# Optimization experiments

Measured on AMD Instinct MI355X. Metric: run time of the kernel, lower is better.

## Reference

```python
import jax, jax.numpy as jnp
import numpy as np

VEC = 64
HEADS = 16
DUP = 4
HIDDEN = VEC * HEADS * DUP  # 4096
EPS = 1e-12


def setup_inputs() -> dict:
    key = jax.random.key(0)
    ks = jax.random.split(key, 7)
    B, S, N = 4, 512, 512
    out_len = VEC * HEADS
    return {
        "embeddings": jax.random.normal(ks[0], (B, S, HIDDEN), jnp.float32),
        "keys": jax.random.normal(ks[1], (B, N, out_len), jnp.float32),
        "values": jax.random.normal(ks[2], (B, N, out_len), jnp.float32),
        "Wq": jax.random.normal(ks[3], (HIDDEN, HIDDEN), jnp.float32) * (1.0 / np.sqrt(HIDDEN)),
        "bq": jnp.zeros((HIDDEN,), jnp.float32),
        "Wre": jax.random.normal(ks[4], (HIDDEN, HIDDEN), jnp.float32) * (1.0 / np.sqrt(HIDDEN)),
        "bre": jnp.zeros((HIDDEN,), jnp.float32),
        "ln_g": jnp.ones((HIDDEN,), jnp.float32),
        "ln_b": jnp.zeros((HIDDEN,), jnp.float32),
    }


def reference(embeddings, keys, values, Wq, bq, Wre, bre, ln_g, ln_b):
    B, S, _ = embeddings.shape
    N = keys.shape[1]
    # query projection: (B,S,hidden) -> reshape to (B, S*DUP, VEC, HEADS) -> (B,H,S*DUP,VEC)
    q = embeddings @ Wq.T + bq
    q = q.reshape(B, S * DUP, VEC, HEADS).transpose(0, 3, 1, 2)
    # keys: (B,N,VEC*HEADS) -> (B,H,VEC,N); values -> (B,H,N,VEC)
    k = keys.reshape(B, N, VEC, HEADS).transpose(0, 3, 2, 1)
    v = values.reshape(B, N, VEC, HEADS).transpose(0, 3, 1, 2)
    scores = jnp.matmul(q, k) / np.sqrt(VEC).astype(np.float32)  # (B,H,S*DUP,N)
    probs = jax.nn.softmax(scores, axis=-1)
    out = jnp.matmul(probs, v)  # (B,H,S*DUP,VEC)
    # (B,H,S*DUP,VEC) -> (B,H,S,VEC*DUP) -> (B,S,H,VEC*DUP) -> (B,S,HIDDEN)
    out = out.reshape(B, HEADS, S, VEC * DUP).transpose(0, 2, 1, 3).reshape(B, S, HIDDEN)
    # LayerNorm (biased variance, torch semantics)
    mu = jnp.mean(out, axis=-1, keepdims=True)
    var = jnp.mean(jnp.square(out - mu), axis=-1, keepdims=True)
    ln = (out - mu) / jnp.sqrt(var + EPS) * ln_g + ln_b
    return ln @ Wre.T + bre
```

## Files before the change

kernel.cpp:

```cpp
#include <hip/hip_runtime.h>

typedef __attribute__((ext_vector_type(8))) _Float16 half8;
typedef __attribute__((ext_vector_type(4))) _Float16 half4;
typedef __attribute__((ext_vector_type(4))) float    floatx4;

#define GLD16(g, l)                                                            \
  __builtin_amdgcn_global_load_lds(                                            \
      (const __attribute__((address_space(1))) void*)(g),                      \
      (__attribute__((address_space(3))) void*)(l), 16, 0, 0)

#define MFMA16(a, b, c) __builtin_amdgcn_mfma_f32_16x16x32_f16(a, b, c, 0, 0, 0)

__device__ __forceinline__ void cvt8(const float* __restrict__ in,
                                     _Float16* __restrict__ out, int i) {
  const float4* p = (const float4*)in + (size_t)i * 2;
  float4 a = p[0], b = p[1];
  half8 h;
  h[0] = (_Float16)a.x; h[1] = (_Float16)a.y; h[2] = (_Float16)a.z; h[3] = (_Float16)a.w;
  h[4] = (_Float16)b.x; h[5] = (_Float16)b.y; h[6] = (_Float16)b.z; h[7] = (_Float16)b.w;
  *(half8*)(out + (size_t)i * 8) = h;
}

__global__ __launch_bounds__(256) void prepA(const float* __restrict__ emb,
                                             const float* __restrict__ Wq,
                                             const float* __restrict__ keys,
                                             const float* __restrict__ values,
                                             _Float16* __restrict__ embH,
                                             _Float16* __restrict__ WqH,
                                             _Float16* __restrict__ Kh,
                                             _Float16* __restrict__ Vt) {
  const int bid = blockIdx.x, t = threadIdx.x;
  if (bid < 4096) {
    cvt8(emb, embH, bid * 256 + t);
  } else if (bid < 12288) {
    cvt8(Wq, WqH, (bid - 4096) * 256 + t);
  } else {
    const int tid = (bid - 12288) * 256 + t;
    {
      int v = tid & 63, n = (tid >> 6) & 511, h = (tid >> 15) & 15, b = tid >> 19;
      Kh[tid] = (_Float16)keys[((size_t)(b * 512 + n)) * 1024 + v * 16 + h];
    }
    {
      int n = tid & 511, v = (tid >> 9) & 63, h = (tid >> 15) & 15, b = tid >> 19;
      Vt[tid] = (_Float16)values[((size_t)(b * 512 + n)) * 1024 + v * 16 + h];
    }
  }
}

template <int MODE>
__global__ __launch_bounds__(512, 2) void gemm_bt(const _Float16* __restrict__ A,
                                                  const _Float16* __restrict__ Bw,
                                                  const float* __restrict__ bias,
                                                  float* __restrict__ Cf,
                                                  _Float16* __restrict__ H0,
                                                  _Float16* __restrict__ H1) {
  const int K = 4096;
  const int NT = 32;
  __shared__ _Float16 lA[2 * 16384];
  __shared__ _Float16 lB[2 * 16384];
  const int t = threadIdx.x, lane = t & 63, w = t >> 6;
  const int m0 = blockIdx.y * 256, n0 = blockIdx.x * 256;
  const int kb = blockIdx.z * 2048;
  const int wm = (w >> 2) * 128, wn = (w & 3) * 64;
  const int fr = lane & 15, fq = lane >> 4;

  const int srow = t >> 3;
  const int sch = (t & 7) ^ (srow & 7);
  const _Float16* gA = A + (size_t)(m0 + srow) * K + kb + sch * 8;
  const _Float16* gB = Bw + (size_t)(n0 + srow) * K + kb + sch * 8;
  _Float16* dA = &lA[t * 8];
  _Float16* dB = &lB[t * 8];

#define STG(op, bf_, kt_, h_)                                                  \
  do {                                                                         \
    const _Float16* g_ = (op ? gB : gA) + (size_t)((h_)*128) * K + (kt_)*64;   \
    _Float16* d_ = (op ? dB : dA) + (bf_)*16384 + (h_)*8192;                   \
    GLD16(g_, d_);                                                             \
    GLD16(g_ + (size_t)64 * K, d_ + 4096);                                     \
  } while (0)

  STG(0, 0, 0, 0); STG(0, 0, 0, 1); STG(1, 0, 0, 0); STG(1, 0, 0, 1);
  STG(0, 1, 1, 0); STG(0, 1, 1, 1); STG(1, 1, 1, 0);
  asm volatile("s_waitcnt vmcnt(6)" ::: "memory");
  __builtin_amdgcn_s_barrier();

  floatx4 acc[8][4];
#pragma unroll
  for (int i = 0; i < 8; i++)
#pragma unroll
    for (int j = 0; j < 4; j++) acc[i][j] = (floatx4)(0.f);

  const _Float16* cA = lA + (wm + fr) * 64;
  const _Float16* cB = lB + (wn + fr) * 64;
  const int xo0 = ((fq) ^ (fr & 7)) * 8;
  const int xo1 = ((4 + fq) ^ (fr & 7)) * 8;

#define QUAD(ibase, jbase)                                                     \
  do {                                                                         \
    __builtin_amdgcn_s_setprio(1);                                             \
    _Pragma("unroll") for (int i_ = 0; i_ < 4; i_++) {                         \
      _Pragma("unroll") for (int jj_ = 0; jj_ < 2; jj_++) {                    \
        acc[(ibase) + i_][(jbase) + jj_] =                                     \
            MFMA16(af[(ibase) + i_][0], bf[jj_][0], acc[(ibase) + i_][(jbase) + jj_]); \
        acc[(ibase) + i_][(jbase) + jj_] =                                     \
            MFMA16(af[(ibase) + i_][1], bf[jj_][1], acc[(ibase) + i_][(jbase) + jj_]); \
      }                                                                        \
    }                                                                          \
    __builtin_amdgcn_s_setprio(0);                                             \
  } while (0)

#define TILE(BUF, TT)                                                          \
  do {                                                                         \
    const int kt1 = ((TT) + 1 < NT) ? (TT) + 1 : NT - 1;                       \
    const int kt2 = ((TT) + 2 < NT) ? (TT) + 2 : NT - 1;                       \
    const int o = (BUF)*16384;                                                 \
    half8 af[8][2], bf[2][2];                                                  \
                              \
    STG(1, (BUF) ^ 1, kt1, 1);                                                 \
    _Pragma("unroll") for (int i = 0; i < 4; i++) {                            \
      af[i][0] = *(const half8*)(cA + o + i * 1024 + xo0);                     \
      af[i][1] = *(const half8*)(cA + o + i * 1024 + xo1);                     \
    }                                                                          \
    _Pragma("unroll") for (int jj = 0; jj < 2; jj++) {                         \
      bf[jj][0] = *(const half8*)(cB + o + jj * 1024 + xo0);                   \
      bf[jj][1] = *(const half8*)(cB + o + jj * 1024 + xo1);                   \
    }                                                                          \
    QUAD(0, 0);                                                                \
    __builtin_amdgcn_s_barrier();                                              \
                                                     \
    _Pragma("unroll") for (int i = 4; i < 8; i++) {                            \
      af[i][0] = *(const half8*)(cA + o + i * 1024 + xo0);                     \
      af[i][1] = *(const half8*)(cA + o + i * 1024 + xo1);                     \
    }                                                                          \
    QUAD(4, 0);                                                                \
    __builtin_amdgcn_s_barrier();                                              \
                                    \
    STG(0, (BUF), kt2, 0);                                                     \
    bf[0][0] = *(const half8*)(cB + o + 2 * 1024 + xo0);                       \
    bf[0][1] = *(const half8*)(cB + o + 2 * 1024 + xo1);                       \
    bf[1][0] = *(const half8*)(cB + o + 3 * 1024 + xo0);                       \
    bf[1][1] = *(const half8*)(cB + o + 3 * 1024 + xo1);                       \
    QUAD(0, 2);                                                                \
    __builtin_amdgcn_s_barrier();                                              \
                        \
    STG(0, (BUF), kt2, 1);                                                     \
    STG(1, (BUF), kt2, 0);                                                     \
    QUAD(4, 2);                                                                \
    asm volatile("s_waitcnt vmcnt(6)" ::: "memory");                           \
    __builtin_amdgcn_s_barrier();                                              \
  } while (0)

  for (int tt = 0; tt < NT; tt += 2) {
    TILE(0, tt);
    TILE(1, tt + 1);
  }

  const int z = blockIdx.z;
#pragma unroll
  for (int i = 0; i < 8; i++)
#pragma unroll
    for (int j = 0; j < 4; j++) {
      const int col = n0 + wn + j * 16 + fr;
      const int rbase = m0 + wm + i * 16 + fq * 4;
      if (MODE == 0 && z == 0) {
        const float bv = bias[col];
#pragma unroll
        for (int r = 0; r < 4; r++)
          Cf[(size_t)(rbase + r) * 4096 + col] = acc[i][j][r] + bv;
      } else {
        _Float16* P = z ? H1 : H0;
#pragma unroll
        for (int r = 0; r < 4; r++)
          P[(size_t)(rbase + r) * 4096 + col] = (_Float16)acc[i][j][r];
      }
    }
#undef TILE
#undef QUAD
#undef STG
}

__global__ __launch_bounds__(256) void prepB(const float* __restrict__ Wre,
                                             _Float16* __restrict__ WreH,
                                             const _Float16* __restrict__ p0,
                                             const _Float16* __restrict__ p1,
                                             const float* __restrict__ bq,
                                             _Float16* __restrict__ q) {
  const int bid = blockIdx.x, t = threadIdx.x;
  if (bid < 8192) {
    cvt8(Wre, WreH, bid * 256 + t);
    return;
  }
  __shared__ _Float16 T[4][16][80];
  const int L = t & 63, w = t >> 6;
  const int m = bid - 8192, d = w;
  const int b = m >> 9, s = m & 511;
  const size_t src = (size_t)m * 4096 + d * 1024 + L * 16;
  half8 a0 = *(const half8*)(p0 + src);
  half8 a1 = *(const half8*)(p0 + src + 8);
  half8 b0 = *(const half8*)(p1 + src);
  half8 b1 = *(const half8*)(p1 + src + 8);
  const float4* bqv = (const float4*)(bq + d * 1024 + L * 16);
  float bias[16];
#pragma unroll
  for (int c = 0; c < 4; c++) {
    float4 f = bqv[c];
    bias[c * 4 + 0] = f.x; bias[c * 4 + 1] = f.y;
    bias[c * 4 + 2] = f.z; bias[c * 4 + 3] = f.w;
  }
#pragma unroll
  for (int h = 0; h < 8; h++) {
    T[w][h][L] = (_Float16)(((float)a0[h] + (float)b0[h] + bias[h]) * 0.125f);
    T[w][h + 8][L] =
        (_Float16)(((float)a1[h] + (float)b1[h] + bias[h + 8]) * 0.125f);
  }
  const int h2 = L >> 2, c2 = L & 3;
  _Float16* dst = q + (((size_t)(b * 16 + h2) * 2048) + s * 4 + d) * 64 + c2 * 8;
  *(half8*)dst = *(const half8*)&T[w][h2][c2 * 8];
  *(half8*)(dst + 32) = *(const half8*)&T[w][h2][32 + c2 * 8];
}

__global__ __launch_bounds__(256) void combine2(float* __restrict__ out,
                                                const _Float16* __restrict__ p1) {
  const int i4 = (blockIdx.x * 256 + threadIdx.x) * 4;
  float4 o = *(float4*)&out[i4];
  half4 p = *(const half4*)(p1 + i4);
  o.x += (float)p[0];
  o.y += (float)p[1];
  o.z += (float)p[2];
  o.w += (float)p[3];
  *(float4*)&out[i4] = o;
}

__global__ __launch_bounds__(256) void attn_mfma(const _Float16* __restrict__ Q,
                                                 const _Float16* __restrict__ Kh,
                                                 const _Float16* __restrict__ Vt,
                                                 float* __restrict__ Out) {
  __shared__ _Float16 Pbuf[4][32][136];
  const int t = threadIdx.x, lane = t & 63, w = t >> 6;
  const int fr = lane & 15, fq = lane >> 4;
  const int bh = blockIdx.y, qt = blockIdx.x;
  const int b = bh >> 4, h = bh & 15;

  const _Float16* Qb = Q + ((size_t)bh * 2048 + qt * 128 + w * 32) * 64;
  const _Float16* Kb = Kh + (size_t)bh * 512 * 64;
  const _Float16* Vb = Vt + (size_t)bh * 64 * 512;

  half8 qf[2][2];
#pragma unroll
  for (int i = 0; i < 2; i++)
#pragma unroll
    for (int ks = 0; ks < 2; ks++)
      qf[i][ks] = *(const half8*)(Qb + (i * 16 + fr) * 64 + ks * 32 + fq * 8);

  floatx4 oacc[2][4];
  float l_acc[2][4];
#pragma unroll
  for (int i = 0; i < 2; i++)
#pragma unroll
    for (int j = 0; j < 4; j++) {
      oacc[i][j] = (floatx4)(0.f);
      l_acc[i][j] = 0.f;
    }

  for (int c0 = 0; c0 < 512; c0 += 128) {
    floatx4 sc[2][8];
#pragma unroll
    for (int i = 0; i < 2; i++)
#pragma unroll
      for (int j = 0; j < 8; j++) sc[i][j] = (floatx4)(0.f);
#pragma unroll
    for (int j = 0; j < 8; j++) {
      const _Float16* kr = Kb + (size_t)(c0 + j * 16 + fr) * 64 + fq * 8;
      half8 k0 = *(const half8*)kr;
      half8 k1 = *(const half8*)(kr + 32);
#pragma unroll
      for (int i = 0; i < 2; i++) {
        sc[i][j] = __builtin_amdgcn_mfma_f32_16x16x32_f16(qf[i][0], k0, sc[i][j], 0, 0, 0);
        sc[i][j] = __builtin_amdgcn_mfma_f32_16x16x32_f16(qf[i][1], k1, sc[i][j], 0, 0, 0);
      }
    }
    half8 vr[4][4];
#pragma unroll
    for (int kn = 0; kn < 4; kn++)
#pragma unroll
      for (int jv = 0; jv < 4; jv++)
        vr[kn][jv] =
            *(const half8*)(Vb + (size_t)(jv * 16 + fr) * 512 + c0 + kn * 32 + fq * 8);
#pragma unroll
    for (int i = 0; i < 2; i++)
#pragma unroll
      for (int j = 0; j < 8; j++)
#pragma unroll
        for (int r = 0; r < 4; r++) {
          float p = __expf(sc[i][j][r]);
          l_acc[i][r] += p;
          Pbuf[w][i * 16 + fq * 4 + r][j * 16 + fr] = (_Float16)p;
        }
#pragma unroll
    for (int kn = 0; kn < 4; kn++) {
      half8 pa[2];
#pragma unroll
      for (int i = 0; i < 2; i++)
        pa[i] = *(const half8*)&Pbuf[w][i * 16 + fr][kn * 32 + fq * 8];
#pragma unroll
      for (int jv = 0; jv < 4; jv++) {
#pragma unroll
        for (int i = 0; i < 2; i++)
          oacc[i][jv] = __builtin_amdgcn_mfma_f32_16x16x32_f16(pa[i], vr[kn][jv],
                                                              oacc[i][jv], 0, 0, 0);
      }
    }
  }

#pragma unroll
  for (int i = 0; i < 2; i++)
#pragma unroll
    for (int r = 0; r < 4; r++) {
#pragma unroll
      for (int m = 8; m; m >>= 1)
        l_acc[i][r] += __shfl_xor(l_acc[i][r], m, 16);
    }
#pragma unroll
  for (int i = 0; i < 2; i++) {
#pragma unroll
    for (int r = 0; r < 4; r++) {
      const float inv = 1.f / l_acc[i][r];
      const int m2 = qt * 128 + w * 32 + i * 16 + fq * 4 + r;
      float* orow = Out + ((size_t)(b * 512 + (m2 >> 2))) * 4096 + h * 256 + (m2 & 3) * 64 + fr;
#pragma unroll
      for (int jv = 0; jv < 4; jv++) orow[jv * 16] = oacc[i][jv][r] * inv;
    }
  }
}

__global__ __launch_bounds__(256) void ln_kernel(const float* __restrict__ X,
                                                 const float* __restrict__ g,
                                                 const float* __restrict__ bb,
                                                 _Float16* __restrict__ Y) {
  const int row = blockIdx.x;
  const int t = threadIdx.x;
  const float* x = X + (size_t)row * 4096;
  float4 vals[4];
  float sum = 0.f, sq = 0.f;
#pragma unroll
  for (int c = 0; c < 4; c++) {
    vals[c] = *(const float4*)&x[c * 1024 + t * 4];
    sum += vals[c].x + vals[c].y + vals[c].z + vals[c].w;
    sq += vals[c].x * vals[c].x + vals[c].y * vals[c].y + vals[c].z * vals[c].z +
          vals[c].w * vals[c].w;
  }
#pragma unroll
  for (int off = 32; off > 0; off >>= 1) {
    sum += __shfl_down(sum, off, 64);
    sq += __shfl_down(sq, off, 64);
  }
  __shared__ float red[8];
  const int w = t >> 6;
  if ((t & 63) == 0) {
    red[w] = sum;
    red[4 + w] = sq;
  }
  __syncthreads();
  sum = red[0] + red[1] + red[2] + red[3];
  sq = red[4] + red[5] + red[6] + red[7];
  const float mu = sum * (1.f / 4096.f);
  float var = sq * (1.f / 4096.f) - mu * mu;
  var = fmaxf(var, 0.f);
  const float rstd = rsqrtf(var + 1e-12f);
#pragma unroll
  for (int c = 0; c < 4; c++) {
    const int j = c * 1024 + t * 4;
    float4 gg = *(const float4*)&g[j];
    float4 bv = *(const float4*)&bb[j];
    half4 y;
    y[0] = (_Float16)((vals[c].x - mu) * rstd * gg.x + bv.x);
    y[1] = (_Float16)((vals[c].y - mu) * rstd * gg.y + bv.y);
    y[2] = (_Float16)((vals[c].z - mu) * rstd * gg.z + bv.z);
    y[3] = (_Float16)((vals[c].w - mu) * rstd * gg.w + bv.w);
    *(half4*)&Y[(size_t)row * 4096 + j] = y;
  }
}

extern "C" void kernel_launch(void* const* d_in, const int* in_sizes, int n_in,
                              void* d_out, int out_size, void* d_ws,
                              size_t ws_size, hipStream_t stream) {
  const float* emb = (const float*)d_in[0];
  const float* keys = (const float*)d_in[1];
  const float* values = (const float*)d_in[2];
  const float* Wq = (const float*)d_in[3];
  const float* bq = (const float*)d_in[4];
  const float* Wre = (const float*)d_in[5];
  const float* bre = (const float*)d_in[6];
  const float* ln_g = (const float*)d_in[7];
  const float* ln_b = (const float*)d_in[8];
  float* out = (float*)d_out;

  char* ws = (char*)d_ws;
  _Float16* embH = (_Float16*)(ws);
  _Float16* WqH = (_Float16*)(ws + ((size_t)16 << 20));
  _Float16* Kh = (_Float16*)(ws + ((size_t)48 << 20));
  _Float16* Vt = (_Float16*)(ws + ((size_t)52 << 20));
  _Float16* P0q = (_Float16*)d_out;
  _Float16* P1q = (_Float16*)((char*)d_out + ((size_t)16 << 20));
  _Float16* WreH = WqH;
  _Float16* qattn = (_Float16*)(ws);
  _Float16* lnH = (_Float16*)(ws + ((size_t)48 << 20));
  _Float16* P1o = (_Float16*)(ws);

  prepA<<<20480, 256, 0, stream>>>(emb, Wq, keys, values, embH, WqH, Kh, Vt);
  gemm_bt<1><<<dim3(16, 8, 2), 512, 0, stream>>>(embH, WqH, nullptr, nullptr,
                                                 P0q, P1q);
  prepB<<<10240, 256, 0, stream>>>(Wre, WreH, P0q, P1q, bq, qattn);
  attn_mfma<<<dim3(16, 64), 256, 0, stream>>>(qattn, Kh, Vt, out);
  ln_kernel<<<2048, 256, 0, stream>>>(out, ln_g, ln_b, lnH);
  gemm_bt<0><<<dim3(16, 8, 2), 512, 0, stream>>>(lnH, WreH, bre, out, nullptr,
                                                 P1o);
  combine2<<<8192, 256, 0, stream>>>(out, P1o);
}
```

Measured before the change: 443.8 us.

## Replace split-K 256x256 GEMM with 128x128 tiles over full K

```diff
diff --git a/kernel.cpp b/kernel.cpp
--- a/kernel.cpp
+++ b/kernel.cpp
@@ -48,45 +48,41 @@
 }
 
 template <int MODE>
-__global__ __launch_bounds__(512, 2) void gemm_bt(const _Float16* __restrict__ A,
+__global__ __launch_bounds__(256, 2) void gemm_bt(const _Float16* __restrict__ A,
                                                   const _Float16* __restrict__ Bw,
                                                   const float* __restrict__ bias,
                                                   float* __restrict__ Cf,
-                                                  _Float16* __restrict__ H0,
-                                                  _Float16* __restrict__ H1) {
+                                                  _Float16* __restrict__ H0) {
   const int K = 4096;
-  const int NT = 32;
-  __shared__ _Float16 lA[2 * 16384];
-  __shared__ _Float16 lB[2 * 16384];
+  const int NT = 64;
+  __shared__ _Float16 lA[2 * 8192];
+  __shared__ _Float16 lB[2 * 8192];
   const int t = threadIdx.x, lane = t & 63, w = t >> 6;
-  const int m0 = blockIdx.y * 256, n0 = blockIdx.x * 256;
-  const int kb = blockIdx.z * 2048;
-  const int wm = (w >> 2) * 128, wn = (w & 3) * 64;
+  const int m0 = blockIdx.y * 128, n0 = blockIdx.x * 128;
+  const int wm = (w >> 1) * 64, wn = (w & 1) * 64;
   const int fr = lane & 15, fq = lane >> 4;
 
   const int srow = t >> 3;
   const int sch = (t & 7) ^ (srow & 7);
-  const _Float16* gA = A + (size_t)(m0 + srow) * K + kb + sch * 8;
-  const _Float16* gB = Bw + (size_t)(n0 + srow) * K + kb + sch * 8;
+  const _Float16* gA = A + (size_t)(m0 + srow) * K + sch * 8;
+  const _Float16* gB = Bw + (size_t)(n0 + srow) * K + sch * 8;
   _Float16* dA = &lA[t * 8];
   _Float16* dB = &lB[t * 8];
 
 #define STG(op, bf_, kt_, h_)                                                  \
-  do {                                                                         \
-    const _Float16* g_ = (op ? gB : gA) + (size_t)((h_)*128) * K + (kt_)*64;   \
-    _Float16* d_ = (op ? dB : dA) + (bf_)*16384 + (h_)*8192;                   \
-    GLD16(g_, d_);                                                             \
-    GLD16(g_ + (size_t)64 * K, d_ + 4096);                                     \
-  } while (0)
-
-  STG(0, 0, 0, 0); STG(0, 0, 0, 1); STG(1, 0, 0, 0); STG(1, 0, 0, 1);
-  STG(0, 1, 1, 0); STG(0, 1, 1, 1); STG(1, 1, 1, 0);
-  asm volatile("s_waitcnt vmcnt(6)" ::: "memory");
+  GLD16((op ? gB : gA) + (size_t)((h_)*32) * K + (kt_)*64,                     \
+        (op ? dB : dA) + (bf_)*8192 + (h_)*2048)
+
+  STG(0, 0, 0, 0); STG(0, 0, 0, 1); STG(0, 0, 0, 2); STG(0, 0, 0, 3);
+  STG(1, 0, 0, 0); STG(1, 0, 0, 1); STG(1, 0, 0, 2); STG(1, 0, 0, 3);
+  STG(0, 1, 1, 0); STG(0, 1, 1, 1); STG(0, 1, 1, 2); STG(0, 1, 1, 3);
+  STG(1, 1, 1, 0); STG(1, 1, 1, 1); STG(1, 1, 1, 2); STG(1, 1, 1, 3);
+  asm volatile("s_waitcnt vmcnt(8)" ::: "memory");
   __builtin_amdgcn_s_barrier();
 
-  floatx4 acc[8][4];
-#pragma unroll
-  for (int i = 0; i < 8; i++)
+  floatx4 acc[4][4];
+#pragma unroll
+  for (int i = 0; i < 4; i++)
 #pragma unroll
     for (int j = 0; j < 4; j++) acc[i][j] = (floatx4)(0.f);
 
@@ -98,12 +94,14 @@
 #define QUAD(ibase, jbase)                                                     \
   do {                                                                         \
     __builtin_amdgcn_s_setprio(1);                                             \
-    _Pragma("unroll") for (int i_ = 0; i_ < 4; i_++) {                         \
+    _Pragma("unroll") for (int i_ = 0; i_ < 2; i_++) {                         \
       _Pragma("unroll") for (int jj_ = 0; jj_ < 2; jj_++) {                    \
-        acc[(ibase) + i_][(jbase) + jj_] =                                     \
-            MFMA16(af[(ibase) + i_][0], bf[jj_][0], acc[(ibase) + i_][(jbase) + jj_]); \
-        acc[(ibase) + i_][(jbase) + jj_] =                                     \
-            MFMA16(af[(ibase) + i_][1], bf[jj_][1], acc[(ibase) + i_][(jbase) + jj_]); \
+        acc[(ibase) + i_][(jbase) + jj_] = MFMA16(                             \
+            af[(ibase) + i_][0], bf[(jbase) + jj_][0],                         \
+            acc[(ibase) + i_][(jbase) + jj_]);                                 \
+        acc[(ibase) + i_][(jbase) + jj_] = MFMA16(                             \
+            af[(ibase) + i_][1], bf[(jbase) + jj_][1],                         \
+            acc[(ibase) + i_][(jbase) + jj_]);                                 \
       }                                                                        \
     }                                                                          \
     __builtin_amdgcn_s_setprio(0);                                             \
@@ -111,42 +109,41 @@
 
 #define TILE(BUF, TT)                                                          \
   do {                                                                         \
-    const int kt1 = ((TT) + 1 < NT) ? (TT) + 1 : NT - 1;                       \
     const int kt2 = ((TT) + 2 < NT) ? (TT) + 2 : NT - 1;                       \
-    const int o = (BUF)*16384;                                                 \
-    half8 af[8][2], bf[2][2];                                                  \
-                              \
-    STG(1, (BUF) ^ 1, kt1, 1);                                                 \
-    _Pragma("unroll") for (int i = 0; i < 4; i++) {                            \
+    const int o = (BUF)*8192;                                                  \
+    half8 af[4][2], bf[4][2];                                                  \
+                                      \
+    _Pragma("unroll") for (int i = 0; i < 2; i++) {                            \
       af[i][0] = *(const half8*)(cA + o + i * 1024 + xo0);                     \
       af[i][1] = *(const half8*)(cA + o + i * 1024 + xo1);                     \
     }                                                                          \
-    _Pragma("unroll") for (int jj = 0; jj < 2; jj++) {                         \
-      bf[jj][0] = *(const half8*)(cB + o + jj * 1024 + xo0);                   \
-      bf[jj][1] = *(const half8*)(cB + o + jj * 1024 + xo1);                   \
+    _Pragma("unroll") for (int j = 0; j < 2; j++) {                            \
+      bf[j][0] = *(const half8*)(cB + o + j * 1024 + xo0);                     \
+      bf[j][1] = *(const half8*)(cB + o + j * 1024 + xo1);                     \
     }                                                                          \
     QUAD(0, 0);                                                                \
     __builtin_amdgcn_s_barrier();                                              \
-                                                     \
-    _Pragma("unroll") for (int i = 4; i < 8; i++) {                            \
+            \
+    STG(0, (BUF), kt2, 0); STG(0, (BUF), kt2, 2);                              \
+    STG(1, (BUF), kt2, 0); STG(1, (BUF), kt2, 2);                              \
+    _Pragma("unroll") for (int i = 2; i < 4; i++) {                            \
       af[i][0] = *(const half8*)(cA + o + i * 1024 + xo0);                     \
       af[i][1] = *(const half8*)(cA + o + i * 1024 + xo1);                     \
     }                                                                          \
-    QUAD(4, 0);                                                                \
+    QUAD(2, 0);                                                                \
     __builtin_amdgcn_s_barrier();                                              \
-                                    \
-    STG(0, (BUF), kt2, 0);                                                     \
-    bf[0][0] = *(const half8*)(cB + o + 2 * 1024 + xo0);                       \
-    bf[0][1] = *(const half8*)(cB + o + 2 * 1024 + xo1);                       \
-    bf[1][0] = *(const half8*)(cB + o + 3 * 1024 + xo0);                       \
-    bf[1][1] = *(const half8*)(cB + o + 3 * 1024 + xo1);                       \
+                      \
+    STG(0, (BUF), kt2, 1); STG(0, (BUF), kt2, 3);                              \
+    _Pragma("unroll") for (int j = 2; j < 4; j++) {                            \
+      bf[j][0] = *(const half8*)(cB + o + j * 1024 + xo0);                     \
+      bf[j][1] = *(const half8*)(cB + o + j * 1024 + xo1);                     \
+    }                                                                          \
     QUAD(0, 2);                                                                \
     __builtin_amdgcn_s_barrier();                                              \
-                        \
-    STG(0, (BUF), kt2, 1);                                                     \
-    STG(1, (BUF), kt2, 0);                                                     \
-    QUAD(4, 2);                                                                \
-    asm volatile("s_waitcnt vmcnt(6)" ::: "memory");                           \
+                       \
+    STG(1, (BUF), kt2, 1); STG(1, (BUF), kt2, 3);                              \
+    QUAD(2, 2);                                                                \
+    asm volatile("s_waitcnt vmcnt(8)" ::: "memory");                           \
     __builtin_amdgcn_s_barrier();                                              \
   } while (0)
 
@@ -155,23 +152,21 @@
     TILE(1, tt + 1);
   }
 
-  const int z = blockIdx.z;
-#pragma unroll
-  for (int i = 0; i < 8; i++)
+#pragma unroll
+  for (int i = 0; i < 4; i++)
 #pragma unroll
     for (int j = 0; j < 4; j++) {
       const int col = n0 + wn + j * 16 + fr;
       const int rbase = m0 + wm + i * 16 + fq * 4;
-      if (MODE == 0 && z == 0) {
+      if (MODE == 0) {
         const float bv = bias[col];
 #pragma unroll
         for (int r = 0; r < 4; r++)
           Cf[(size_t)(rbase + r) * 4096 + col] = acc[i][j][r] + bv;
       } else {
-        _Float16* P = z ? H1 : H0;
 #pragma unroll
         for (int r = 0; r < 4; r++)
-          P[(size_t)(rbase + r) * 4096 + col] = (_Float16)acc[i][j][r];
+          H0[(size_t)(rbase + r) * 4096 + col] = (_Float16)acc[i][j][r];
       }
     }
 #undef TILE
@@ -182,7 +177,6 @@
 __global__ __launch_bounds__(256) void prepB(const float* __restrict__ Wre,
                                              _Float16* __restrict__ WreH,
                                              const _Float16* __restrict__ p0,
-                                             const _Float16* __restrict__ p1,
                                              const float* __restrict__ bq,
                                              _Float16* __restrict__ q) {
   const int bid = blockIdx.x, t = threadIdx.x;
@@ -197,8 +191,6 @@
   const size_t src = (size_t)m * 4096 + d * 1024 + L * 16;
   half8 a0 = *(const half8*)(p0 + src);
   half8 a1 = *(const half8*)(p0 + src + 8);
-  half8 b0 = *(const half8*)(p1 + src);
-  half8 b1 = *(const half8*)(p1 + src + 8);
   const float4* bqv = (const float4*)(bq + d * 1024 + L * 16);
   float bias[16];
 #pragma unroll
@@ -209,26 +201,13 @@
   }
 #pragma unroll
   for (int h = 0; h < 8; h++) {
-    T[w][h][L] = (_Float16)(((float)a0[h] + (float)b0[h] + bias[h]) * 0.125f);
-    T[w][h + 8][L] =
-        (_Float16)(((float)a1[h] + (float)b1[h] + bias[h + 8]) * 0.125f);
+    T[w][h][L] = (_Float16)(((float)a0[h] + bias[h]) * 0.125f);
+    T[w][h + 8][L] = (_Float16)(((float)a1[h] + bias[h + 8]) * 0.125f);
   }
   const int h2 = L >> 2, c2 = L & 3;
   _Float16* dst = q + (((size_t)(b * 16 + h2) * 2048) + s * 4 + d) * 64 + c2 * 8;
   *(half8*)dst = *(const half8*)&T[w][h2][c2 * 8];
   *(half8*)(dst + 32) = *(const half8*)&T[w][h2][32 + c2 * 8];
-}
-
-__global__ __launch_bounds__(256) void combine2(float* __restrict__ out,
-                                                const _Float16* __restrict__ p1) {
-  const int i4 = (blockIdx.x * 256 + threadIdx.x) * 4;
-  float4 o = *(float4*)&out[i4];
-  half4 p = *(const half4*)(p1 + i4);
-  o.x += (float)p[0];
-  o.y += (float)p[1];
-  o.z += (float)p[2];
-  o.w += (float)p[3];
-  *(float4*)&out[i4] = o;
 }
 
 __global__ __launch_bounds__(256) void attn_mfma(const _Float16* __restrict__ Q,
@@ -401,19 +380,14 @@
   _Float16* Kh = (_Float16*)(ws + ((size_t)48 << 20));
   _Float16* Vt = (_Float16*)(ws + ((size_t)52 << 20));
   _Float16* P0q = (_Float16*)d_out;
-  _Float16* P1q = (_Float16*)((char*)d_out + ((size_t)16 << 20));
   _Float16* WreH = WqH;
   _Float16* qattn = (_Float16*)(ws);
   _Float16* lnH = (_Float16*)(ws + ((size_t)48 << 20));
-  _Float16* P1o = (_Float16*)(ws);
 
   prepA<<<20480, 256, 0, stream>>>(emb, Wq, keys, values, embH, WqH, Kh, Vt);
-  gemm_bt<1><<<dim3(16, 8, 2), 512, 0, stream>>>(embH, WqH, nullptr, nullptr,
-                                                 P0q, P1q);
-  prepB<<<10240, 256, 0, stream>>>(Wre, WreH, P0q, P1q, bq, qattn);
+  gemm_bt<1><<<dim3(32, 16), 256, 0, stream>>>(embH, WqH, nullptr, nullptr, P0q);
+  prepB<<<10240, 256, 0, stream>>>(Wre, WreH, P0q, bq, qattn);
   attn_mfma<<<dim3(16, 64), 256, 0, stream>>>(qattn, Kh, Vt, out);
   ln_kernel<<<2048, 256, 0, stream>>>(out, ln_g, ln_b, lnH);
-  gemm_bt<0><<<dim3(16, 8, 2), 512, 0, stream>>>(lnH, WreH, bre, out, nullptr,
-                                                 P1o);
-  combine2<<<8192, 256, 0, stream>>>(out, P1o);
-}
+  gemm_bt<0><<<dim3(32, 16), 256, 0, stream>>>(lnH, WreH, bre, out, nullptr);
+}
```

New measurement: 431.4 us. 1.03x faster.
